# Kernel tuning notes

Measured on AMD Instinct MI355X. Metric: run time of the kernel, lower is better.

## Reference

```python
import jax, jax.numpy as jnp
import numpy as np

N = 50000
E = 1600000
IN = 128
HID = 128
OUT = 64
NL = 200000
NEG_SLOPE = 0.2


def _glorot(key, shape):
    fan_in, fan_out = shape[0], shape[-1]
    s = jnp.sqrt(6.0 / (fan_in + fan_out))
    return jax.random.uniform(key, shape, jnp.float32, -s, s)


def setup_inputs() -> dict:
    key = jax.random.key(0)
    ks = jax.random.split(key, 16)
    x = jax.random.normal(ks[0], (N, IN), jnp.float32)
    edge_index = jax.random.randint(ks[1], (2, E), 0, N, dtype=jnp.int32)
    edge_label_index = jax.random.randint(ks[2], (2, NL), 0, N, dtype=jnp.int32)
    return {
        "x": x,
        "edge_index": edge_index,
        "edge_label_index": edge_label_index,
        "W1": _glorot(ks[3], (IN, HID)),  "a1s": _glorot(ks[4], (HID,)),  "a1d": _glorot(ks[5], (HID,)),  "b1": jnp.zeros((HID,), jnp.float32),
        "W2": _glorot(ks[6], (HID, HID)), "a2s": _glorot(ks[7], (HID,)),  "a2d": _glorot(ks[8], (HID,)),  "b2": jnp.zeros((HID,), jnp.float32),
        "W3": _glorot(ks[9], (HID, HID)), "a3s": _glorot(ks[10], (HID,)), "a3d": _glorot(ks[11], (HID,)), "b3": jnp.zeros((HID,), jnp.float32),
        "W4": _glorot(ks[12], (HID, OUT)), "b4": jnp.zeros((OUT,), jnp.float32),
    }


def _add_self_loops(edge_index, n):
    loop = jnp.arange(n, dtype=edge_index.dtype)
    return jnp.concatenate([edge_index, jnp.stack([loop, loop])], axis=1)


def gat_conv(x, edge_index, W, a_s, a_d, b):
    """PyG GATConv, heads=1, add_self_loops=True: gather, LeakyReLU score,
    segment softmax over destination nodes, scatter-add aggregate."""
    n = x.shape[0]
    ei = _add_self_loops(edge_index, n)
    src, dst = ei[0], ei[1]
    h = x @ W                                    # [N, H]
    e = jax.nn.leaky_relu((h @ a_s)[src] + (h @ a_d)[dst], NEG_SLOPE)  # [E']
    m = jax.ops.segment_max(e, dst, num_segments=n)
    p = jnp.exp(e - m[dst])
    s = jax.ops.segment_sum(p, dst, num_segments=n)
    alpha = p / s[dst]                           # segment softmax
    out = jax.ops.segment_sum(h[src] * alpha[:, None], dst, num_segments=n)
    return out + b


def gcn_conv(x, edge_index, W, b):
    """PyG GCNConv: self-loops + symmetric degree normalization."""
    n = x.shape[0]
    ei = _add_self_loops(edge_index, n)
    src, dst = ei[0], ei[1]
    h = x @ W
    deg = jax.ops.segment_sum(jnp.ones(src.shape, h.dtype), dst, num_segments=n)
    dinv = jax.lax.rsqrt(deg)
    norm = dinv[src] * dinv[dst]                 # [E']
    out = jax.ops.segment_sum(h[src] * norm[:, None], dst, num_segments=n)
    return out + b


def reference(x, edge_index, edge_label_index,
              W1, a1s, a1d, b1, W2, a2s, a2d, b2,
              W3, a3s, a3d, b3, W4, b4):
    h = jax.nn.relu(gat_conv(x, edge_index, W1, a1s, a1d, b1))
    h = jax.nn.relu(gat_conv(h, edge_index, W2, a2s, a2d, b2))
    h = jax.nn.relu(gat_conv(h, edge_index, W3, a3s, a3d, b3))
    z = gcn_conv(h, edge_index, W4, b4)          # [N, OUT]
    # decode: dot product of endpoint embeddings -> link logits [NL]
    return (z[edge_label_index[0]] * z[edge_label_index[1]]).sum(axis=-1)
```

## Files before the change

kernel.cpp:

```cpp
#include <hip/hip_runtime.h>
#include <hip/hip_fp16.h>
#include <math.h>

#define NN   50000
#define NE   1600000
#define NLBL 200000
#define CAP  80
#define NEG  0.2f
#define NBK  196
#define CAPB 8800
#define CHK  4096
#define GBIN 391

typedef unsigned short u16;
typedef _Float16 half8 __attribute__((ext_vector_type(8)));
typedef float floatx4 __attribute__((ext_vector_type(4)));
typedef unsigned int u32x4 __attribute__((ext_vector_type(4)));


__device__ void ph_bin(int blk, const int* __restrict__ ei,
                       int* __restrict__ gcnt, unsigned* __restrict__ bins) {
    __shared__ int cntL[NBK];
    __shared__ int offL[NBK];
    __shared__ int curL[NBK];
    __shared__ int curG[NBK];
    __shared__ unsigned stage[CHK];
    const int tid = threadIdx.x;
    const int e0 = blk * CHK + tid * 16;
    const bool act = (e0 + 15) < NE;

    unsigned pk[16];
    int bb[16];
    if (act) {
#pragma unroll
        for (int g = 0; g < 4; ++g) {
            int4 s4 = *(const int4*)&ei[e0 + g * 4];
            int4 d4 = *(const int4*)&ei[NE + e0 + g * 4];
            int sa[4] = {s4.x, s4.y, s4.z, s4.w};
            int da[4] = {d4.x, d4.y, d4.z, d4.w};
#pragma unroll
            for (int k = 0; k < 4; ++k) {
                int idx = g * 4 + k;
                bb[idx] = da[k] >> 8;
                pk[idx] = (unsigned)sa[k] | ((unsigned)(da[k] & 255) << 16)
                        | ((unsigned)bb[idx] << 24);
            }
        }
    }
    for (int i = tid; i < NBK; i += 256) cntL[i] = 0;
    __syncthreads();
    if (act) {
#pragma unroll
        for (int k = 0; k < 16; ++k) atomicAdd(&cntL[bb[k]], 1);
    }
    __syncthreads();
    if (tid < NBK) {
        int acc = 0;
        for (int i = 0; i < tid; ++i) acc += cntL[i];
        offL[tid] = acc;
        curL[tid] = acc;
    }
    __syncthreads();
    for (int i = tid; i < NBK; i += 256) curG[i] = atomicAdd(&gcnt[i], cntL[i]);
    __syncthreads();
    if (act) {
#pragma unroll
        for (int k = 0; k < 16; ++k) {
            int pos = atomicAdd(&curL[bb[k]], 1);
            stage[pos] = pk[k];
        }
    }
    __syncthreads();
    const int tot = offL[NBK - 1] + cntL[NBK - 1];
    for (int j = tid; j < tot; j += 256) {
        unsigned v = stage[j];
        int b = v >> 24;
        int lr = j - offL[b];
        bins[(size_t)b * CAPB + curG[b] + lr] = v & 0x00FFFFFFu;
    }
}

__global__ __launch_bounds__(256) void k_build(const unsigned* __restrict__ bins,
                                               const int* __restrict__ gcnt,
                                               int* __restrict__ cnt,
                                               u16* __restrict__ csr) {
    __shared__ u16 rows[256 * CAP];
    __shared__ int cur[256];
    const int b = blockIdx.x, tid = threadIdx.x;
    const int d0 = b << 8;
    const int nd = min(256, NN - d0);
    if (tid < nd) { cur[tid] = 1; rows[tid * CAP] = (u16)(d0 + tid); }
    __syncthreads();
    const int n = gcnt[b];
    for (int i = tid; i < n; i += 256) {
        unsigned v = bins[(size_t)b * CAPB + i];
        int s = v & 0xFFFF, dl = (v >> 16) & 0xFF;
        int pos = atomicAdd(&cur[dl], 1);
        if (pos < CAP) rows[dl * CAP + pos] = (u16)s;
    }
    __syncthreads();
    const unsigned* rw = (const unsigned*)rows;
    unsigned* cw = (unsigned*)(csr + (size_t)d0 * CAP);
    const int tot = nd * (CAP / 2);
    for (int i = tid; i < tot; i += 256) cw[i] = rw[i];
    if (tid < nd) cnt[d0 + tid] = cur[tid];
}


__global__ __launch_bounds__(256) void k_pre(const float* __restrict__ W1f,
                                             const float* __restrict__ W2f,
                                             const float* __restrict__ W3f,
                                             const float* __restrict__ W4f,
                                             half8* __restrict__ Wf1,
                                             half8* __restrict__ Wf2,
                                             half8* __restrict__ Wf3,
                                             half8* __restrict__ Wf4,
                                             int* __restrict__ gcnt) {
    if (blockIdx.x == 28) {
        int i = threadIdx.x;
        if (i < NBK) gcnt[i] = 0;
        return;
    }
    int e = blockIdx.x * 256 + threadIdx.x;
    const float* W;
    half8* Wf;
    int nout, le;
    if (e < 2048)      { W = W1f; Wf = Wf1; nout = 128; le = e; }
    else if (e < 4096) { W = W2f; Wf = Wf2; nout = 128; le = e - 2048; }
    else if (e < 6144) { W = W3f; Wf = Wf3; nout = 128; le = e - 4096; }
    else               { W = W4f; Wf = Wf4; nout = 64;  le = e - 6144; }
    int c = le >> 8, rem = le & 255, ks = rem >> 6, lane = rem & 63;
    int n = lane & 15, quad = lane >> 4;
    int col = c * 16 + n, k0 = ks * 32 + quad * 8;
    half8 v;
#pragma unroll
    for (int j = 0; j < 8; ++j) v[j] = (_Float16)W[(size_t)(k0 + j) * nout + col];
    Wf[le] = v;
}


template <int NOUT, bool ATTN, typename TA>
__device__ __forceinline__ void gemm_tile(int gt, int lane,
                                          const TA* __restrict__ A0,
                                          const TA* __restrict__ A1,
                                          const half8* __restrict__ Wf,
                                          __half* __restrict__ C0,
                                          __half* __restrict__ C1,
                                          const float* __restrict__ a_s,
                                          const float* __restrict__ a_d,
                                          float* __restrict__ asv,
                                          float* __restrict__ adv) {
    constexpr int CT = NOUT / 16;
    const int n = lane & 15, quad = lane >> 4;
    if (gt * 16 >= NN) return;
    const int row = gt * 16 + n;

    half8 a[4];
#pragma unroll
    for (int ks = 0; ks < 4; ++ks) {
        int c128 = ks * 32 + quad * 8;
        if constexpr (sizeof(TA) == 2) {
            const TA* Ah = (c128 < 64) ? A0 : A1;
            a[ks] = *(const half8*)((const _Float16*)Ah + (size_t)row * 64 + (c128 & 63));
        } else {
            const float* Ap = (const float*)A0 + (size_t)row * 128 + c128;
            float4 f0 = *(const float4*)Ap;
            float4 f1 = *(const float4*)(Ap + 4);
            half8 v;
            v[0] = (_Float16)f0.x; v[1] = (_Float16)f0.y; v[2] = (_Float16)f0.z; v[3] = (_Float16)f0.w;
            v[4] = (_Float16)f1.x; v[5] = (_Float16)f1.y; v[6] = (_Float16)f1.z; v[7] = (_Float16)f1.w;
            a[ks] = v;
        }
    }

    floatx4 acc[CT];
#pragma unroll
    for (int c = 0; c < CT; ++c) acc[c] = (floatx4){0.f, 0.f, 0.f, 0.f};
#pragma unroll
    for (int c = 0; c < CT; ++c) {
#pragma unroll
        for (int ks = 0; ks < 4; ++ks) {
            half8 b = Wf[(c * 4 + ks) * 64 + lane];
            acc[c] = __builtin_amdgcn_mfma_f32_16x16x32_f16(b, a[ks], acc[c], 0, 0, 0);
        }
    }

#pragma unroll
    for (int c = 0; c < CT; ++c) {
        __half* Ch = (NOUT == 64 || c < 4) ? C0 : C1;
        int coff = (NOUT == 64 || c < 4) ? c * 16 : (c - 4) * 16;
        __half2 h0 = __floats2half2_rn(acc[c][0], acc[c][1]);
        __half2 h1 = __floats2half2_rn(acc[c][2], acc[c][3]);
        uint2 u;
        __builtin_memcpy(&u.x, &h0, 4);
        __builtin_memcpy(&u.y, &h1, 4);
        *(uint2*)&Ch[(size_t)row * 64 + coff + quad * 4] = u;
    }

    if (ATTN) {
        float ps = 0.f, pd = 0.f;
#pragma unroll
        for (int c = 0; c < CT; ++c) {
#pragma unroll
            for (int reg = 0; reg < 4; ++reg) {
                float w = acc[c][reg];
                ps = fmaf(w, a_s[c * 16 + quad * 4 + reg], ps);
                pd = fmaf(w, a_d[c * 16 + quad * 4 + reg], pd);
            }
        }
        ps += __shfl_xor(ps, 16); ps += __shfl_xor(ps, 32);
        pd += __shfl_xor(pd, 16); pd += __shfl_xor(pd, 32);
        if (quad == 0) { asv[row] = ps; adv[row] = pd; }
    }
}

__global__ __launch_bounds__(256) void k_bin_gemm1(const int* __restrict__ ei,
                                                   int* __restrict__ gcnt,
                                                   unsigned* __restrict__ bins,
                                                   const float* __restrict__ x,
                                                   const half8* __restrict__ Wf1,
                                                   __half* __restrict__ G0,
                                                   __half* __restrict__ G1,
                                                   const float* __restrict__ a_s,
                                                   const float* __restrict__ a_d,
                                                   float* __restrict__ asv,
                                                   float* __restrict__ adv) {
    if (blockIdx.x < GBIN) { ph_bin(blockIdx.x, ei, gcnt, bins); return; }
    int gt = (blockIdx.x - GBIN) * 4 + (threadIdx.x >> 6);
    gemm_tile<128, true, float>(gt, threadIdx.x & 63, x, x, Wf1, G0, G1, a_s, a_d, asv, adv);
}

template <int NOUT, bool ATTN>
__global__ __launch_bounds__(64) void k_gemm64(const __half* __restrict__ A0,
                                               const __half* __restrict__ A1,
                                               const half8* __restrict__ Wf,
                                               __half* __restrict__ C0,
                                               __half* __restrict__ C1,
                                               const float* __restrict__ a_s,
                                               const float* __restrict__ a_d,
                                               float* __restrict__ asv,
                                               float* __restrict__ adv) {
    gemm_tile<NOUT, ATTN, __half>(blockIdx.x, threadIdx.x & 63, A0, A1, Wf, C0, C1,
                                  a_s, a_d, asv, adv);
}

__device__ __forceinline__ void fma_h8v(half8 h, float al, float* acc) {
#pragma unroll
    for (int k = 0; k < 8; ++k) acc[k] = fmaf(al, (float)h[k], acc[k]);
}


__global__ __launch_bounds__(256) void k_gat_agg(const __half* __restrict__ h0,
                                                 const __half* __restrict__ h1,
                                                 const int* __restrict__ cnt,
                                                 const u16* __restrict__ csr,
                                                 const float* __restrict__ asv,
                                                 const float* __restrict__ adv,
                                                 const float* __restrict__ bias,
                                                 __half* __restrict__ out0,
                                                 __half* __restrict__ out1) {
    __shared__ float alsL[4][88];
    __shared__ int   srcL[4][88];
    int lane = threadIdx.x & 63, wv = threadIdx.x >> 6;
    int d = blockIdx.x * 4 + wv;
    if (d >= NN) return;
    int deg = cnt[d]; if (deg > CAP) deg = CAP;
    const float advd = adv[d];
    const u16* rowp = csr + (size_t)d * CAP;

    int j0 = lane, j1 = lane + 64;
    int s0 = 0, s1 = 0;
    float e0 = -INFINITY, e1 = -INFINITY;
    if (j0 < deg) {
        s0 = rowp[j0];
        float t = asv[s0] + advd;
        e0 = (t >= 0.f) ? t : NEG * t;
    }
    if (j1 < deg) {
        s1 = rowp[j1];
        float t = asv[s1] + advd;
        e1 = (t >= 0.f) ? t : NEG * t;
    }
    float m = fmaxf(e0, e1);
#pragma unroll
    for (int off = 32; off; off >>= 1) m = fmaxf(m, __shfl_xor(m, off));
    float p0 = (j0 < deg) ? __expf(e0 - m) : 0.f;
    float p1 = (j1 < deg) ? __expf(e1 - m) : 0.f;
    float s = p0 + p1;
#pragma unroll
    for (int off = 32; off; off >>= 1) s += __shfl_xor(s, off);
    float inv = 1.f / s;
    alsL[wv][j0] = p0 * inv;
    srcL[wv][j0] = s0;
    if (j1 < 88) { alsL[wv][j1] = p1 * inv; srcL[wv][j1] = s1; }

    int slot = lane >> 3, r = lane & 7;
    int degp = (deg + 7) & ~7;
#pragma unroll
    for (int half = 0; half < 2; ++half) {
        const __half* ht = half ? h1 : h0;
        __half* ot = half ? out1 : out0;
        float acc[8];
#pragma unroll
        for (int k = 0; k < 8; ++k) acc[k] = 0.f;

        for (int base = 0; base < degp; base += 8) {
            int idx = base + slot;
            float al = alsL[wv][idx];
            int   sj = srcL[wv][idx];
            half8 hv = *(const half8*)&ht[(size_t)sj * 64 + r * 8];
            fma_h8v(hv, al, acc);
        }
#pragma unroll
        for (int k = 0; k < 8; ++k) {
            acc[k] += __shfl_xor(acc[k], 8);
            acc[k] += __shfl_xor(acc[k], 16);
            acc[k] += __shfl_xor(acc[k], 32);
        }
        if (slot == 0) {
            __half2 ho[4];
#pragma unroll
            for (int k = 0; k < 4; ++k) {
                float oa = fmaxf(acc[2 * k]     + bias[half * 64 + r * 8 + 2 * k],     0.f);
                float ob = fmaxf(acc[2 * k + 1] + bias[half * 64 + r * 8 + 2 * k + 1], 0.f);
                ho[k] = __floats2half2_rn(oa, ob);
            }
            u32x4 u;
            __builtin_memcpy(&u, &ho[0], 16);
            __builtin_nontemporal_store(u, (u32x4*)&ot[(size_t)d * 64 + r * 8]);
        }
    }
}


__global__ __launch_bounds__(256) void k_gcn_agg(const __half* __restrict__ h,
                                                 const int* __restrict__ cnt,
                                                 const u16* __restrict__ csr,
                                                 const float* __restrict__ bias,
                                                 __half* __restrict__ z) {
    __shared__ float nmL[4][88];
    __shared__ int   srcL[4][88];
    int lane = threadIdx.x & 63, wv = threadIdx.x >> 6;
    int d = blockIdx.x * 4 + wv;
    if (d >= NN) return;
    int degc = cnt[d];
    int deg = degc > CAP ? CAP : degc;
    float did = rsqrtf((float)degc);
    const u16* rowp = csr + (size_t)d * CAP;

    int j0 = lane, j1 = lane + 64;
    int s0 = 0, s1 = 0;
    float n0 = 0.f, n1 = 0.f;
    if (j0 < deg) { s0 = rowp[j0]; n0 = rsqrtf((float)cnt[s0]) * did; }
    if (j1 < deg) { s1 = rowp[j1]; n1 = rsqrtf((float)cnt[s1]) * did; }
    nmL[wv][j0] = n0;
    srcL[wv][j0] = s0;
    if (j1 < 88) { nmL[wv][j1] = n1; srcL[wv][j1] = s1; }

    int slot = lane >> 3, r = lane & 7;
    float acc[8];
#pragma unroll
    for (int k = 0; k < 8; ++k) acc[k] = 0.f;

    int degp = (deg + 7) & ~7;
    for (int base = 0; base < degp; base += 8) {
        int idx = base + slot;
        float nm = nmL[wv][idx];
        int   sj = srcL[wv][idx];
        half8 hv = *(const half8*)&h[(size_t)sj * 64 + r * 8];
        fma_h8v(hv, nm, acc);
    }
#pragma unroll
    for (int k = 0; k < 8; ++k) {
        acc[k] += __shfl_xor(acc[k], 8);
        acc[k] += __shfl_xor(acc[k], 16);
        acc[k] += __shfl_xor(acc[k], 32);
    }
    if (slot == 0) {
        __half2 ho[4];
#pragma unroll
        for (int k = 0; k < 4; ++k) {
            float oa = acc[2 * k]     + bias[r * 8 + 2 * k];
            float ob = acc[2 * k + 1] + bias[r * 8 + 2 * k + 1];
            ho[k] = __floats2half2_rn(oa, ob);
        }
        uint4 u;
        __builtin_memcpy(&u, &ho[0], 16);
        *(uint4*)&z[(size_t)d * 64 + r * 8] = u;
    }
}


__global__ __launch_bounds__(256) void k_decode(const __half* __restrict__ z,
                                                const int* __restrict__ eli,
                                                float* __restrict__ outp) {
    int lane = threadIdx.x & 63, wv = threadIdx.x >> 6;
    int g = lane >> 4, r = lane & 15;
    int idx = (blockIdx.x * 4 + wv) * 4 + g;
    if (idx >= NLBL) return;
    int a = eli[idx], b = eli[NLBL + idx];
    uint2 ua = *(const uint2*)&z[(size_t)a * 64 + r * 4];
    uint2 ub = *(const uint2*)&z[(size_t)b * 64 + r * 4];
    float2 a0 = __half22float2(*(__half2*)&ua.x);
    float2 a1 = __half22float2(*(__half2*)&ua.y);
    float2 b0 = __half22float2(*(__half2*)&ub.x);
    float2 b1 = __half22float2(*(__half2*)&ub.y);
    float v = a0.x * b0.x + a0.y * b0.y + a1.x * b1.x + a1.y * b1.y;
#pragma unroll
    for (int off = 8; off; off >>= 1) v += __shfl_xor(v, off);
    if (r == 0) outp[idx] = v;
}


extern "C" void kernel_launch(void* const* d_in, const int* in_sizes, int n_in,
                              void* d_out, int out_size, void* d_ws, size_t ws_size,
                              hipStream_t stream) {
    const float* x   = (const float*)d_in[0];
    const int*   ei  = (const int*)d_in[1];
    const int*   eli = (const int*)d_in[2];
    const float* W1 = (const float*)d_in[3];
    const float* a1s = (const float*)d_in[4];
    const float* a1d = (const float*)d_in[5];
    const float* b1 = (const float*)d_in[6];
    const float* W2 = (const float*)d_in[7];
    const float* a2s = (const float*)d_in[8];
    const float* a2d = (const float*)d_in[9];
    const float* b2 = (const float*)d_in[10];
    const float* W3 = (const float*)d_in[11];
    const float* a3s = (const float*)d_in[12];
    const float* a3d = (const float*)d_in[13];
    const float* b3 = (const float*)d_in[14];
    const float* W4 = (const float*)d_in[15];
    const float* b4 = (const float*)d_in[16];
    float* outp = (float*)d_out;

    char* p = (char*)d_ws;
    auto alloc = [&](size_t bytes) -> char* {
        char* r = p;
        p += (bytes + 255) & ~(size_t)255;
        return r;
    };
    int*    cnt  = (int*)alloc((size_t)NN * 4);
    u16*    csr  = (u16*)alloc((size_t)NN * CAP * 2);
    int*    gcnt = (int*)alloc((size_t)NBK * 4);
    float*  asv  = (float*)alloc((size_t)NN * 4);
    float*  advv = (float*)alloc((size_t)NN * 4);
    __half* G0   = (__half*)alloc((size_t)NN * 64 * 2);
    __half* G1   = (__half*)alloc((size_t)NN * 64 * 2);
    __half* B1a  = (__half*)alloc((size_t)NN * 64 * 2);
    __half* B1b  = (__half*)alloc((size_t)NN * 64 * 2);
    __half* B2a  = (__half*)alloc((size_t)NN * 64 * 2);
    __half* B2b  = (__half*)alloc((size_t)NN * 64 * 2);
    __half* zf   = (__half*)alloc((size_t)NN * 64 * 2);
    half8*  Wf1  = (half8*)alloc(2048 * 16);
    half8*  Wf2  = (half8*)alloc(2048 * 16);
    half8*  Wf3  = (half8*)alloc(2048 * 16);
    half8*  Wf4  = (half8*)alloc(1024 * 16);
    unsigned* bins = (unsigned*)alloc((size_t)NBK * CAPB * 4);

    const int gG1   = GBIN + 782;
    const int gGemm = (NN + 15) / 16;
    const int gNode = (NN + 3) / 4;
    const int gDec  = (NLBL + 15) / 16;

    k_pre<<<29, 256, 0, stream>>>(W1, W2, W3, W4, Wf1, Wf2, Wf3, Wf4, gcnt);
    k_bin_gemm1<<<gG1, 256, 0, stream>>>(ei, gcnt, bins, x, Wf1, G0, G1, a1s, a1d, asv, advv);
    k_build<<<NBK, 256, 0, stream>>>(bins, gcnt, cnt, csr);

    k_gat_agg<<<gNode, 256, 0, stream>>>(G0, G1, cnt, csr, asv, advv, b1, B1a, B1b);

    k_gemm64<128, true><<<gGemm, 64, 0, stream>>>(B1a, B1b, Wf2, G0, G1, a2s, a2d, asv, advv);
    k_gat_agg<<<gNode, 256, 0, stream>>>(G0, G1, cnt, csr, asv, advv, b2, B2a, B2b);

    k_gemm64<128, true><<<gGemm, 64, 0, stream>>>(B2a, B2b, Wf3, G0, G1, a3s, a3d, asv, advv);
    k_gat_agg<<<gNode, 256, 0, stream>>>(G0, G1, cnt, csr, asv, advv, b3, B1a, B1b);

    k_gemm64<64, false><<<gGemm, 64, 0, stream>>>(B1a, B1b, Wf4, G0, G0, nullptr, nullptr, nullptr, nullptr);
    k_gcn_agg<<<gNode, 256, 0, stream>>>(G0, cnt, csr, b4, zf);

    k_decode<<<gDec, 256, 0, stream>>>(zf, eli, outp);
}
```

Baseline: 373.7 us.

## Fuse GAT aggregation with the next layer's GEMM and attention projections

```diff
diff --git a/kernel.cpp b/kernel.cpp
--- a/kernel.cpp
+++ b/kernel.cpp
@@ -15,7 +15,6 @@
 typedef unsigned short u16;
 typedef _Float16 half8 __attribute__((ext_vector_type(8)));
 typedef float floatx4 __attribute__((ext_vector_type(4)));
-typedef unsigned int u32x4 __attribute__((ext_vector_type(4)));
 
 
 __device__ void ph_bin(int blk, const int* __restrict__ ei,
@@ -139,18 +138,15 @@
 }
 
 
-template <int NOUT, bool ATTN, typename TA>
-__device__ __forceinline__ void gemm_tile(int gt, int lane,
-                                          const TA* __restrict__ A0,
-                                          const TA* __restrict__ A1,
-                                          const half8* __restrict__ Wf,
-                                          __half* __restrict__ C0,
-                                          __half* __restrict__ C1,
-                                          const float* __restrict__ a_s,
-                                          const float* __restrict__ a_d,
-                                          float* __restrict__ asv,
-                                          float* __restrict__ adv) {
-    constexpr int CT = NOUT / 16;
+__device__ __forceinline__ void gemm1_tile(int gt, int lane,
+                                           const float* __restrict__ x,
+                                           const half8* __restrict__ Wf,
+                                           __half* __restrict__ C0,
+                                           __half* __restrict__ C1,
+                                           const float* __restrict__ a_s,
+                                           const float* __restrict__ a_d,
+                                           float* __restrict__ asv,
+                                           float* __restrict__ adv) {
     const int n = lane & 15, quad = lane >> 4;
     if (gt * 16 >= NN) return;
     const int row = gt * 16 + n;
@@ -158,26 +154,20 @@
     half8 a[4];
 #pragma unroll
     for (int ks = 0; ks < 4; ++ks) {
-        int c128 = ks * 32 + quad * 8;
-        if constexpr (sizeof(TA) == 2) {
-            const TA* Ah = (c128 < 64) ? A0 : A1;
-            a[ks] = *(const half8*)((const _Float16*)Ah + (size_t)row * 64 + (c128 & 63));
-        } else {
-            const float* Ap = (const float*)A0 + (size_t)row * 128 + c128;
-            float4 f0 = *(const float4*)Ap;
-            float4 f1 = *(const float4*)(Ap + 4);
-            half8 v;
-            v[0] = (_Float16)f0.x; v[1] = (_Float16)f0.y; v[2] = (_Float16)f0.z; v[3] = (_Float16)f0.w;
-            v[4] = (_Float16)f1.x; v[5] = (_Float16)f1.y; v[6] = (_Float16)f1.z; v[7] = (_Float16)f1.w;
-            a[ks] = v;
-        }
-    }
-
-    floatx4 acc[CT];
-#pragma unroll
-    for (int c = 0; c < CT; ++c) acc[c] = (floatx4){0.f, 0.f, 0.f, 0.f};
-#pragma unroll
-    for (int c = 0; c < CT; ++c) {
+        const float* Ap = x + (size_t)row * 128 + ks * 32 + quad * 8;
+        float4 f0 = *(const float4*)Ap;
+        float4 f1 = *(const float4*)(Ap + 4);
+        half8 v;
+        v[0] = (_Float16)f0.x; v[1] = (_Float16)f0.y; v[2] = (_Float16)f0.z; v[3] = (_Float16)f0.w;
+        v[4] = (_Float16)f1.x; v[5] = (_Float16)f1.y; v[6] = (_Float16)f1.z; v[7] = (_Float16)f1.w;
+        a[ks] = v;
+    }
+
+    floatx4 acc[8];
+#pragma unroll
+    for (int c = 0; c < 8; ++c) acc[c] = (floatx4){0.f, 0.f, 0.f, 0.f};
+#pragma unroll
+    for (int c = 0; c < 8; ++c) {
 #pragma unroll
         for (int ks = 0; ks < 4; ++ks) {
             half8 b = Wf[(c * 4 + ks) * 64 + lane];
@@ -186,9 +176,9 @@
     }
 
 #pragma unroll
-    for (int c = 0; c < CT; ++c) {
-        __half* Ch = (NOUT == 64 || c < 4) ? C0 : C1;
-        int coff = (NOUT == 64 || c < 4) ? c * 16 : (c - 4) * 16;
+    for (int c = 0; c < 8; ++c) {
+        __half* Ch = (c < 4) ? C0 : C1;
+        int coff = (c < 4) ? c * 16 : (c - 4) * 16;
         __half2 h0 = __floats2half2_rn(acc[c][0], acc[c][1]);
         __half2 h1 = __floats2half2_rn(acc[c][2], acc[c][3]);
         uint2 u;
@@ -197,21 +187,19 @@
         *(uint2*)&Ch[(size_t)row * 64 + coff + quad * 4] = u;
     }
 
-    if (ATTN) {
-        float ps = 0.f, pd = 0.f;
-#pragma unroll
-        for (int c = 0; c < CT; ++c) {
-#pragma unroll
-            for (int reg = 0; reg < 4; ++reg) {
-                float w = acc[c][reg];
-                ps = fmaf(w, a_s[c * 16 + quad * 4 + reg], ps);
-                pd = fmaf(w, a_d[c * 16 + quad * 4 + reg], pd);
-            }
-        }
-        ps += __shfl_xor(ps, 16); ps += __shfl_xor(ps, 32);
-        pd += __shfl_xor(pd, 16); pd += __shfl_xor(pd, 32);
-        if (quad == 0) { asv[row] = ps; adv[row] = pd; }
-    }
+    float ps = 0.f, pd = 0.f;
+#pragma unroll
+    for (int c = 0; c < 8; ++c) {
+#pragma unroll
+        for (int reg = 0; reg < 4; ++reg) {
+            float w = acc[c][reg];
+            ps = fmaf(w, a_s[c * 16 + quad * 4 + reg], ps);
+            pd = fmaf(w, a_d[c * 16 + quad * 4 + reg], pd);
+        }
+    }
+    ps += __shfl_xor(ps, 16); ps += __shfl_xor(ps, 32);
+    pd += __shfl_xor(pd, 16); pd += __shfl_xor(pd, 32);
+    if (quad == 0) { asv[row] = ps; adv[row] = pd; }
 }
 
 __global__ __launch_bounds__(256) void k_bin_gemm1(const int* __restrict__ ei,
@@ -227,21 +215,7 @@
                                                    float* __restrict__ adv) {
     if (blockIdx.x < GBIN) { ph_bin(blockIdx.x, ei, gcnt, bins); return; }
     int gt = (blockIdx.x - GBIN) * 4 + (threadIdx.x >> 6);
-    gemm_tile<128, true, float>(gt, threadIdx.x & 63, x, x, Wf1, G0, G1, a_s, a_d, asv, adv);
-}
-
-template <int NOUT, bool ATTN>
-__global__ __launch_bounds__(64) void k_gemm64(const __half* __restrict__ A0,
-                                               const __half* __restrict__ A1,
-                                               const half8* __restrict__ Wf,
-                                               __half* __restrict__ C0,
-                                               __half* __restrict__ C1,
-                                               const float* __restrict__ a_s,
-                                               const float* __restrict__ a_d,
-                                               float* __restrict__ asv,
-                                               float* __restrict__ adv) {
-    gemm_tile<NOUT, ATTN, __half>(blockIdx.x, threadIdx.x & 63, A0, A1, Wf, C0, C1,
-                                  a_s, a_d, asv, adv);
+    gemm1_tile(gt, threadIdx.x & 63, x, Wf1, G0, G1, a_s, a_d, asv, adv);
 }
 
 __device__ __forceinline__ void fma_h8v(half8 h, float al, float* acc) {
@@ -250,84 +224,131 @@
 }
 
 
-__global__ __launch_bounds__(256) void k_gat_agg(const __half* __restrict__ h0,
-                                                 const __half* __restrict__ h1,
-                                                 const int* __restrict__ cnt,
-                                                 const u16* __restrict__ csr,
-                                                 const float* __restrict__ asv,
-                                                 const float* __restrict__ adv,
-                                                 const float* __restrict__ bias,
-                                                 __half* __restrict__ out0,
-                                                 __half* __restrict__ out1) {
+template <int NOUT2, bool ATTN2>
+__global__ __launch_bounds__(256) void k_gat_fused(const __half* __restrict__ h0,
+                                                   const __half* __restrict__ h1,
+                                                   const int* __restrict__ cnt,
+                                                   const u16* __restrict__ csr,
+                                                   const float* __restrict__ asv_in,
+                                                   const float* __restrict__ adv_in,
+                                                   const float* __restrict__ bias,
+                                                   const half8* __restrict__ WfN,
+                                                   const float* __restrict__ a_sN,
+                                                   const float* __restrict__ a_dN,
+                                                   float* __restrict__ asvN,
+                                                   float* __restrict__ advN,
+                                                   __half* __restrict__ GO0,
+                                                   __half* __restrict__ GO1) {
     __shared__ float alsL[4][88];
     __shared__ int   srcL[4][88];
-    int lane = threadIdx.x & 63, wv = threadIdx.x >> 6;
-    int d = blockIdx.x * 4 + wv;
-    if (d >= NN) return;
-    int deg = cnt[d]; if (deg > CAP) deg = CAP;
-    const float advd = adv[d];
-    const u16* rowp = csr + (size_t)d * CAP;
-
-    int j0 = lane, j1 = lane + 64;
-    int s0 = 0, s1 = 0;
-    float e0 = -INFINITY, e1 = -INFINITY;
-    if (j0 < deg) {
-        s0 = rowp[j0];
-        float t = asv[s0] + advd;
-        e0 = (t >= 0.f) ? t : NEG * t;
-    }
-    if (j1 < deg) {
-        s1 = rowp[j1];
-        float t = asv[s1] + advd;
-        e1 = (t >= 0.f) ? t : NEG * t;
-    }
-    float m = fmaxf(e0, e1);
-#pragma unroll
-    for (int off = 32; off; off >>= 1) m = fmaxf(m, __shfl_xor(m, off));
-    float p0 = (j0 < deg) ? __expf(e0 - m) : 0.f;
-    float p1 = (j1 < deg) ? __expf(e1 - m) : 0.f;
-    float s = p0 + p1;
-#pragma unroll
-    for (int off = 32; off; off >>= 1) s += __shfl_xor(s, off);
-    float inv = 1.f / s;
-    alsL[wv][j0] = p0 * inv;
-    srcL[wv][j0] = s0;
-    if (j1 < 88) { alsL[wv][j1] = p1 * inv; srcL[wv][j1] = s1; }
-
-    int slot = lane >> 3, r = lane & 7;
-    int degp = (deg + 7) & ~7;
-#pragma unroll
-    for (int half = 0; half < 2; ++half) {
-        const __half* ht = half ? h1 : h0;
-        __half* ot = half ? out1 : out0;
-        float acc[8];
-#pragma unroll
-        for (int k = 0; k < 8; ++k) acc[k] = 0.f;
-
-        for (int base = 0; base < degp; base += 8) {
-            int idx = base + slot;
-            float al = alsL[wv][idx];
-            int   sj = srcL[wv][idx];
-            half8 hv = *(const half8*)&ht[(size_t)sj * 64 + r * 8];
-            fma_h8v(hv, al, acc);
-        }
-#pragma unroll
-        for (int k = 0; k < 8; ++k) {
-            acc[k] += __shfl_xor(acc[k], 8);
-            acc[k] += __shfl_xor(acc[k], 16);
-            acc[k] += __shfl_xor(acc[k], 32);
-        }
-        if (slot == 0) {
-            __half2 ho[4];
-#pragma unroll
-            for (int k = 0; k < 4; ++k) {
-                float oa = fmaxf(acc[2 * k]     + bias[half * 64 + r * 8 + 2 * k],     0.f);
-                float ob = fmaxf(acc[2 * k + 1] + bias[half * 64 + r * 8 + 2 * k + 1], 0.f);
-                ho[k] = __floats2half2_rn(oa, ob);
+    __shared__ _Float16 Bs[16][136];
+    __shared__ float psL[16], pdL[16];
+    const int lane = threadIdx.x & 63, wv = threadIdx.x >> 6;
+    const int d0 = blockIdx.x * 16;
+    if (ATTN2 && threadIdx.x < 16) { psL[threadIdx.x] = 0.f; pdL[threadIdx.x] = 0.f; }
+
+    for (int it = 0; it < 4; ++it) {
+        const int d = d0 + wv * 4 + it;
+        int deg = cnt[d]; if (deg > CAP) deg = CAP;
+        const float advd = adv_in[d];
+        const u16* rowp = csr + (size_t)d * CAP;
+
+        int j0 = lane, j1 = lane + 64;
+        int s0 = 0, s1 = 0;
+        float e0 = -INFINITY, e1 = -INFINITY;
+        if (j0 < deg) {
+            s0 = rowp[j0];
+            float t = asv_in[s0] + advd;
+            e0 = (t >= 0.f) ? t : NEG * t;
+        }
+        if (j1 < deg) {
+            s1 = rowp[j1];
+            float t = asv_in[s1] + advd;
+            e1 = (t >= 0.f) ? t : NEG * t;
+        }
+        float m = fmaxf(e0, e1);
+#pragma unroll
+        for (int off = 32; off; off >>= 1) m = fmaxf(m, __shfl_xor(m, off));
+        float p0 = (j0 < deg) ? __expf(e0 - m) : 0.f;
+        float p1 = (j1 < deg) ? __expf(e1 - m) : 0.f;
+        float s = p0 + p1;
+#pragma unroll
+        for (int off = 32; off; off >>= 1) s += __shfl_xor(s, off);
+        float inv = 1.f / s;
+        alsL[wv][j0] = p0 * inv;
+        srcL[wv][j0] = s0;
+        if (j1 < 88) { alsL[wv][j1] = p1 * inv; srcL[wv][j1] = s1; }
+
+        int slot = lane >> 3, r = lane & 7;
+        int degp = (deg + 7) & ~7;
+#pragma unroll
+        for (int half = 0; half < 2; ++half) {
+            const __half* ht = half ? h1 : h0;
+            float acc[8];
+#pragma unroll
+            for (int k = 0; k < 8; ++k) acc[k] = 0.f;
+            for (int base = 0; base < degp; base += 8) {
+                int idx = base + slot;
+                float al = alsL[wv][idx];
+                int   sj = srcL[wv][idx];
+                half8 hv = *(const half8*)&ht[(size_t)sj * 64 + r * 8];
+                fma_h8v(hv, al, acc);
             }
-            u32x4 u;
-            __builtin_memcpy(&u, &ho[0], 16);
-            __builtin_nontemporal_store(u, (u32x4*)&ot[(size_t)d * 64 + r * 8]);
+#pragma unroll
+            for (int k = 0; k < 8; ++k) {
+                acc[k] += __shfl_xor(acc[k], 8);
+                acc[k] += __shfl_xor(acc[k], 16);
+                acc[k] += __shfl_xor(acc[k], 32);
+            }
+            if (slot == 0) {
+                _Float16* bp = &Bs[wv * 4 + it][half * 64 + r * 8];
+#pragma unroll
+                for (int k = 0; k < 8; ++k)
+                    bp[k] = (_Float16)fmaxf(acc[k] + bias[half * 64 + r * 8 + k], 0.f);
+            }
+        }
+    }
+    __syncthreads();
+
+    constexpr int CTW = (NOUT2 == 128) ? 2 : 1;
+    const int n = lane & 15, quad = lane >> 4;
+    const int row = d0 + n;
+    float ps = 0.f, pd = 0.f;
+#pragma unroll
+    for (int ct = 0; ct < CTW; ++ct) {
+        const int c = wv * CTW + ct;
+        floatx4 acc2 = (floatx4){0.f, 0.f, 0.f, 0.f};
+#pragma unroll
+        for (int ks = 0; ks < 4; ++ks) {
+            half8 b = *(const half8*)&Bs[n][ks * 32 + quad * 8];
+            half8 a = WfN[(c * 4 + ks) * 64 + lane];
+            acc2 = __builtin_amdgcn_mfma_f32_16x16x32_f16(a, b, acc2, 0, 0, 0);
+        }
+        __half* Ch = (NOUT2 == 64 || c < 4) ? GO0 : GO1;
+        int coff = (NOUT2 == 64 || c < 4) ? c * 16 : (c - 4) * 16;
+        __half2 h0p = __floats2half2_rn(acc2[0], acc2[1]);
+        __half2 h1p = __floats2half2_rn(acc2[2], acc2[3]);
+        uint2 u;
+        __builtin_memcpy(&u.x, &h0p, 4);
+        __builtin_memcpy(&u.y, &h1p, 4);
+        *(uint2*)&Ch[(size_t)row * 64 + coff + quad * 4] = u;
+        if (ATTN2) {
+#pragma unroll
+            for (int reg = 0; reg < 4; ++reg) {
+                float w = acc2[reg];
+                ps = fmaf(w, a_sN[c * 16 + quad * 4 + reg], ps);
+                pd = fmaf(w, a_dN[c * 16 + quad * 4 + reg], pd);
+            }
+        }
+    }
+    if (ATTN2) {
+        ps += __shfl_xor(ps, 16); ps += __shfl_xor(ps, 32);
+        pd += __shfl_xor(pd, 16); pd += __shfl_xor(pd, 32);
+        if (quad == 0) { atomicAdd(&psL[n], ps); atomicAdd(&pdL[n], pd); }
+        __syncthreads();
+        if (threadIdx.x < 16) {
+            asvN[d0 + threadIdx.x] = psL[threadIdx.x];
+            advN[d0 + threadIdx.x] = pdL[threadIdx.x];
         }
     }
 }
@@ -443,14 +464,15 @@
     int*    cnt  = (int*)alloc((size_t)NN * 4);
     u16*    csr  = (u16*)alloc((size_t)NN * CAP * 2);
     int*    gcnt = (int*)alloc((size_t)NBK * 4);
-    float*  asv  = (float*)alloc((size_t)NN * 4);
-    float*  advv = (float*)alloc((size_t)NN * 4);
+    float*  asvA = (float*)alloc((size_t)NN * 4);
+    float*  advA = (float*)alloc((size_t)NN * 4);
+    float*  asvB = (float*)alloc((size_t)NN * 4);
+    float*  advB = (float*)alloc((size_t)NN * 4);
     __half* G0   = (__half*)alloc((size_t)NN * 64 * 2);
     __half* G1   = (__half*)alloc((size_t)NN * 64 * 2);
-    __half* B1a  = (__half*)alloc((size_t)NN * 64 * 2);
-    __half* B1b  = (__half*)alloc((size_t)NN * 64 * 2);
-    __half* B2a  = (__half*)alloc((size_t)NN * 64 * 2);
-    __half* B2b  = (__half*)alloc((size_t)NN * 64 * 2);
+    __half* H0   = (__half*)alloc((size_t)NN * 64 * 2);
+    __half* H1   = (__half*)alloc((size_t)NN * 64 * 2);
+    __half* Z0   = (__half*)alloc((size_t)NN * 64 * 2);
     __half* zf   = (__half*)alloc((size_t)NN * 64 * 2);
     half8*  Wf1  = (half8*)alloc(2048 * 16);
     half8*  Wf2  = (half8*)alloc(2048 * 16);
@@ -459,24 +481,21 @@
     unsigned* bins = (unsigned*)alloc((size_t)NBK * CAPB * 4);
 
     const int gG1   = GBIN + 782;
-    const int gGemm = (NN + 15) / 16;
+    const int gFus  = NN / 16;
     const int gNode = (NN + 3) / 4;
     const int gDec  = (NLBL + 15) / 16;
 
     k_pre<<<29, 256, 0, stream>>>(W1, W2, W3, W4, Wf1, Wf2, Wf3, Wf4, gcnt);
-    k_bin_gemm1<<<gG1, 256, 0, stream>>>(ei, gcnt, bins, x, Wf1, G0, G1, a1s, a1d, asv, advv);
+    k_bin_gemm1<<<gG1, 256, 0, stream>>>(ei, gcnt, bins, x, Wf1, G0, G1, a1s, a1d, asvA, advA);
     k_build<<<NBK, 256, 0, stream>>>(bins, gcnt, cnt, csr);
 
-    k_gat_agg<<<gNode, 256, 0, stream>>>(G0, G1, cnt, csr, asv, advv, b1, B1a, B1b);
-
-    k_gemm64<128, true><<<gGemm, 64, 0, stream>>>(B1a, B1b, Wf2, G0, G1, a2s, a2d, asv, advv);
-    k_gat_agg<<<gNode, 256, 0, stream>>>(G0, G1, cnt, csr, asv, advv, b2, B2a, B2b);
-
-    k_gemm64<128, true><<<gGemm, 64, 0, stream>>>(B2a, B2b, Wf3, G0, G1, a3s, a3d, asv, advv);
-    k_gat_agg<<<gNode, 256, 0, stream>>>(G0, G1, cnt, csr, asv, advv, b3, B1a, B1b);
-
-    k_gemm64<64, false><<<gGemm, 64, 0, stream>>>(B1a, B1b, Wf4, G0, G0, nullptr, nullptr, nullptr, nullptr);
-    k_gcn_agg<<<gNode, 256, 0, stream>>>(G0, cnt, csr, b4, zf);
-
+    k_gat_fused<128, true><<<gFus, 256, 0, stream>>>(G0, G1, cnt, csr, asvA, advA, b1,
+                                                     Wf2, a2s, a2d, asvB, advB, H0, H1);
+    k_gat_fused<128, true><<<gFus, 256, 0, stream>>>(H0, H1, cnt, csr, asvB, advB, b2,
+                                                     Wf3, a3s, a3d, asvA, advA, G0, G1);
+    k_gat_fused<64, false><<<gFus, 256, 0, stream>>>(G0, G1, cnt, csr, asvA, advA, b3,
+                                                     Wf4, nullptr, nullptr, nullptr, nullptr,
+                                                     Z0, Z0);
+    k_gcn_agg<<<gNode, 256, 0, stream>>>(Z0, cnt, csr, b4, zf);
     k_decode<<<gDec, 256, 0, stream>>>(zf, eli, outp);
 }
```

Result: slower. 383.2 us (+2.6%).
